# Kernel optimization log

Hardware: AMD Instinct MI355X
Metric: run time of the kernel (lower is better)

The kernel has to match this reference:

```python
import jax, jax.numpy as jnp
from jax import lax
import numpy as np

N_INPUTS = 2048
UNITS = 2048
L = 8
FANIN = 4096
TOTAL = N_INPUTS + L * UNITS  # 18432, size of flattened outputs vector


def setup_inputs() -> dict:
    key = jax.random.key(0)
    k1, k2, k3, k4 = jax.random.split(key, 4)
    x = jax.random.normal(k1, (N_INPUTS,), dtype=jnp.float32)
    node_inds = jax.random.randint(k2, (L, FANIN), 0, TOTAL, dtype=jnp.int32)
    # 0.02 scale keeps tanh out of deep saturation (matches small evolved weights)
    Ws = jax.random.normal(k3, (L, FANIN, UNITS), dtype=jnp.float32) * 0.02
    bs = jax.random.normal(k4, (L, UNITS), dtype=jnp.float32) * 0.02
    return {"x": x, "node_inds": node_inds, "Ws": Ws, "bs": bs}


def reference(x, node_inds, Ws, bs):
    # Flattened shared state vector, zero-initialized like the tf.Variable.
    outputs = jnp.zeros((TOTAL,), dtype=x.dtype)
    start = 0  # static python offset: out_update_inds are contiguous ranges
    for i in range(L):
        # scatter_nd_update of x into contiguous slice == dynamic_update_slice
        outputs = lax.dynamic_update_slice(outputs, x, (start,))
        start += x.shape[0]
        # gather node-specific indices then tiny Dense + tanh
        gathered = jnp.take(outputs, node_inds[i])          # [FANIN]
        x = jnp.tanh(gathered @ Ws[i] + bs[i])              # [UNITS]
    return x
```

## Files before the change

kernel.cpp:

```cpp
#include <hip/hip_runtime.h>
#include <cmath>

#define N_INPUTS 2048
#define UNITS    2048
#define L_LAYERS 8
#define FANIN    4096
#define TOTAL    18432

#define NTHREADS 256
#define RK       16
#define KC       (FANIN / RK)
#define JTILE    1024
#define P_BLOCKS (2 * KC)

__global__ __launch_bounds__(NTHREADS) void init_kernel(
    const float* __restrict__ x, float* __restrict__ outputs)
{
    int gtid = blockIdx.x * NTHREADS + threadIdx.x;
    if (gtid < TOTAL)
        outputs[gtid] = (gtid < N_INPUTS) ? x[gtid] : 0.0f;
}

__global__ __launch_bounds__(NTHREADS) void p_kernel(
    int layer,
    const int*   __restrict__ node_inds,
    const float* __restrict__ Ws,
    const float* __restrict__ outputs,
    float*       __restrict__ partials)
{
    const int b = blockIdx.x;
    const int t = threadIdx.x;
    const int jhalf = b & 1;
    const int kc    = b >> 1;

    __shared__ float gsh[RK];
    if (t < RK) {
        int idx = node_inds[layer * FANIN + kc * RK + t];
        gsh[t] = outputs[idx];
    }
    __syncthreads();

    const int jbase = jhalf * JTILE + t * 4;
    const float4* W4 = (const float4*)(
        Ws + ((size_t)layer * FANIN + (size_t)kc * RK) * UNITS + jbase);

    float4 a; a.x = 0.f; a.y = 0.f; a.z = 0.f; a.w = 0.f;
    #pragma unroll
    for (int k = 0; k < RK; ++k) {
        float  g = gsh[k];
        float4 w = W4[(size_t)k * (UNITS / 4)];
        a.x += g * w.x; a.y += g * w.y; a.z += g * w.z; a.w += g * w.w;
    }
    *(float4*)(partials + (size_t)kc * UNITS + jbase) = a;
}

__global__ __launch_bounds__(NTHREADS) void f_kernel(
    int layer,
    const float* __restrict__ partials,
    const float* __restrict__ bs,
    float*       __restrict__ outputs,
    float*       __restrict__ out)
{
    int col = blockIdx.x * NTHREADS + threadIdx.x;
    float s = 0.f;
    #pragma unroll 8
    for (int m = 0; m < KC; ++m)
        s += partials[(size_t)m * UNITS + col];
    float y = tanhf(s + bs[layer * UNITS + col]);
    if (layer == L_LAYERS - 1) out[col] = y;
    else outputs[(layer + 1) * UNITS + col] = y;
}

extern "C" void kernel_launch(void* const* d_in, const int* in_sizes, int n_in,
                              void* d_out, int out_size, void* d_ws, size_t ws_size,
                              hipStream_t stream) {
    const float* x         = (const float*)d_in[0];
    const int*   node_inds = (const int*)  d_in[1];
    const float* Ws        = (const float*)d_in[2];
    const float* bs        = (const float*)d_in[3];
    float*       out       = (float*)d_out;
    float*       ws        = (float*)d_ws;

    float* outputs  = ws;
    float* partials = ws + TOTAL;

    init_kernel<<<(TOTAL + NTHREADS - 1) / NTHREADS, NTHREADS, 0, stream>>>(
        x, outputs);

    for (int i = 0; i < L_LAYERS; ++i) {
        p_kernel<<<P_BLOCKS, NTHREADS, 0, stream>>>(
            i, node_inds, Ws, outputs, partials);
        f_kernel<<<UNITS / NTHREADS, NTHREADS, 0, stream>>>(
            i, partials, bs, outputs, out);
    }
}
```

Measured before the change: 496.6 us.

## Fuse partial-sum reduction and tanh into next layer's matvec kernel

Removes the separate init and finalize kernels. Each layer kernel now reduces the previous layer's partial sums with wave-level shuffles: every block writes four output columns, and gathered indices that fall in the just-computed layer are recomputed on demand. Partial buffers are double-buffered so a layer can read the previous partials while writing new ones. This cuts kernel launches from 17 to 9, at the cost of redundant column reductions (each a 256-element strided read) inside every block.

New measurement: 416.9 us. -16.0%, faster.

```diff
diff --git a/kernel.cpp b/kernel.cpp
--- a/kernel.cpp
+++ b/kernel.cpp
@@ -13,30 +13,66 @@
 #define JTILE    1024
 #define P_BLOCKS (2 * KC)
 
-__global__ __launch_bounds__(NTHREADS) void init_kernel(
-    const float* __restrict__ x, float* __restrict__ outputs)
+__device__ __forceinline__ float col_reduce(const float* __restrict__ P, int col)
 {
-    int gtid = blockIdx.x * NTHREADS + threadIdx.x;
-    if (gtid < TOTAL)
-        outputs[gtid] = (gtid < N_INPUTS) ? x[gtid] : 0.0f;
+    int lane = threadIdx.x & 63;
+    float s = 0.f;
+    #pragma unroll
+    for (int m = 0; m < KC / 64; ++m)
+        s += P[(size_t)(lane + m * 64) * UNITS + col];
+    #pragma unroll
+    for (int off = 32; off; off >>= 1)
+        s += __shfl_down(s, off, 64);
+    return __shfl(s, 0, 64);
 }
 
-__global__ __launch_bounds__(NTHREADS) void p_kernel(
+__global__ __launch_bounds__(NTHREADS) void layer_kernel(
     int layer,
+    const float* __restrict__ x,
     const int*   __restrict__ node_inds,
     const float* __restrict__ Ws,
-    const float* __restrict__ outputs,
-    float*       __restrict__ partials)
+    const float* __restrict__ bs,
+    float*       __restrict__ outputs,
+    const float* __restrict__ Pprev,
+    float*       __restrict__ Pcur)
 {
-    const int b = blockIdx.x;
-    const int t = threadIdx.x;
+    const int b    = blockIdx.x;
+    const int t    = threadIdx.x;
+    const int wv   = t >> 6;
+    const int lane = t & 63;
     const int jhalf = b & 1;
     const int kc    = b >> 1;
 
     __shared__ float gsh[RK];
-    if (t < RK) {
-        int idx = node_inds[layer * FANIN + kc * RK + t];
-        gsh[t] = outputs[idx];
+
+    {
+        int col = b * 4 + wv;
+        if (layer == 0) {
+            if (lane == 0) outputs[col] = x[col];
+        } else {
+            float s = col_reduce(Pprev, col);
+            float y = tanhf(s + bs[(layer - 1) * UNITS + col]);
+            if (lane == 0) outputs[(size_t)layer * UNITS + col] = y;
+        }
+    }
+
+    #pragma unroll
+    for (int j = 0; j < 4; ++j) {
+        int q   = wv * 4 + j;
+        int idx = node_inds[layer * FANIN + kc * RK + q];
+        float g;
+        if (layer == 0) {
+            g = (idx < N_INPUTS) ? x[idx] : 0.f;
+        } else if (idx < layer * UNITS) {
+            g = outputs[idx];
+        } else if (idx < (layer + 1) * UNITS) {
+            int col = idx - layer * UNITS;
+            float s = col_reduce(Pprev, col);
+            g = tanhf(s + bs[(layer - 1) * UNITS + col]);
+        } else {
+            g = 0.f;
+        }
+        if (lane == 0) gsh[q] = g;
     }
     __syncthreads();
 
@@ -51,24 +87,20 @@
         float4 w = W4[(size_t)k * (UNITS / 4)];
         a.x += g * w.x; a.y += g * w.y; a.z += g * w.z; a.w += g * w.w;
     }
-    *(float4*)(partials + (size_t)kc * UNITS + jbase) = a;
+    *(float4*)(Pcur + (size_t)kc * UNITS + jbase) = a;
 }
 
-__global__ __launch_bounds__(NTHREADS) void f_kernel(
-    int layer,
-    const float* __restrict__ partials,
+__global__ __launch_bounds__(NTHREADS) void tail_kernel(
+    const float* __restrict__ Pprev,
     const float* __restrict__ bs,
-    float*       __restrict__ outputs,
     float*       __restrict__ out)
 {
-    int col = blockIdx.x * NTHREADS + threadIdx.x;
-    float s = 0.f;
-    #pragma unroll 8
-    for (int m = 0; m < KC; ++m)
-        s += partials[(size_t)m * UNITS + col];
-    float y = tanhf(s + bs[layer * UNITS + col]);
-    if (layer == L_LAYERS - 1) out[col] = y;
-    else outputs[(layer + 1) * UNITS + col] = y;
+    int wv   = threadIdx.x >> 6;
+    int lane = threadIdx.x & 63;
+    int col  = blockIdx.x * 4 + wv;
+    float s = col_reduce(Pprev, col);
+    float y = tanhf(s + bs[(L_LAYERS - 1) * UNITS + col]);
+    if (lane == 0) out[col] = y;
 }
 
 extern "C" void kernel_launch(void* const* d_in, const int* in_sizes, int n_in,
@@ -81,16 +113,18 @@
     float*       out       = (float*)d_out;
     float*       ws        = (float*)d_ws;
 
-    float* outputs  = ws;
-    float* partials = ws + TOTAL;
+    float* outputs = ws;
+    float* P0      = ws + TOTAL;
+    float* P1      = P0 + (size_t)KC * UNITS;
 
-    init_kernel<<<(TOTAL + NTHREADS - 1) / NTHREADS, NTHREADS, 0, stream>>>(
-        x, outputs);
+    float* pbuf[2] = { P0, P1 };
 
     for (int i = 0; i < L_LAYERS; ++i) {
-        p_kernel<<<P_BLOCKS, NTHREADS, 0, stream>>>(
-            i, node_inds, Ws, outputs, partials);
-        f_kernel<<<UNITS / NTHREADS, NTHREADS, 0, stream>>>(
-            i, partials, bs, outputs, out);
+        layer_kernel<<<P_BLOCKS, NTHREADS, 0, stream>>>(
+            i, x, node_inds, Ws, bs, outputs,
+            pbuf[(i + 1) & 1],
+            pbuf[i & 1]);
     }
+    tail_kernel<<<UNITS / 4, NTHREADS, 0, stream>>>(
+        pbuf[(L_LAYERS - 1) & 1], bs, out);
 }
```
